# Kernel optimization log

Hardware: AMD Instinct MI355X
Metric: run time of the kernel (lower is better)

Reference implementation:

```python
import jax, jax.numpy as jnp
import numpy as np


def setup_inputs() -> dict:
    key = jax.random.key(0)
    k1, k2 = jax.random.split(key)
    b, n, d, c, h = 8, 2048, 512, 8192, 1
    x = jax.random.normal(k1, (b, n, d), dtype=jnp.float32)
    # codebook buffer: l2norm(uniform_init(h, c, d)) -- unit-norm rows
    embed = jax.random.normal(k2, (h, c, d), dtype=jnp.float32)
    embed = embed / jnp.linalg.norm(embed, axis=-1, keepdims=True)
    return {"x": x, "embed": embed}


def reference(x, embed):
    # x: [b, n, d] (ndim < 4 -> prepend codebook dim h=1); embed: [h, c, d]
    h = embed.shape[0]
    b, n, d = x.shape
    flatten = x.astype(jnp.float32).reshape(h, b * n, d)   # pack 'h * d'
    # cosine-sim scores (x assumed pre-l2-normalized via transform_input upstream)
    dist = jnp.einsum('hnd,hcd->hnc', flatten, embed)      # [h, b*n, c]
    # gumbel_sample at inference / temp->argmax: deterministic argmax over codes
    embed_ind = jnp.argmax(dist, axis=-1)                  # [h, b*n]
    ind = embed_ind.reshape(h, b, n)                       # unpack 'h *'
    # batched_embedding: gather codebook rows per index -> [h, b, n, d]
    quantize = embed[jnp.arange(h)[:, None, None], ind]
    dist = dist.reshape(h, b, n, -1)                       # unpack 'h * d'
    # needs_codebook_dim: squeeze h=1 on quantize and embed_ind (dist keeps h)
    return quantize[0], ind[0], dist
```

## Files before the change

kernel.cpp:

```cpp
#include <hip/hip_runtime.h>


#define NROWS   16384
#define NCOLS   8192
#define KDIM    512
#define KSPLIT  1024
#define NCTILES 64

#define BM 128
#define BN 128
#define BK 32
#define NSTEPS 48

typedef float f32x4 __attribute__((ext_vector_type(4)));
typedef short s16x8 __attribute__((ext_vector_type(8)));

static __device__ __forceinline__ unsigned short f2bf_rne(float f) {
    unsigned u = __float_as_uint(f);
    u = (u + 0x7FFFu + ((u >> 16) & 1u)) >> 16;
    return (unsigned short)u;
}
static __device__ __forceinline__ float bf2f(unsigned short h) {
    return __uint_as_float(((unsigned)h) << 16);
}

#define GLOAD_LDS16(g, l)                                                              \
    __builtin_amdgcn_global_load_lds((const __attribute__((address_space(1))) void*)(g), \
                                     (__attribute__((address_space(3))) void*)(l), 16, 0, 0)

__global__ __launch_bounds__(128) void split_kernel(
    const float* __restrict__ x, const float* __restrict__ embed,
    unsigned short* __restrict__ A, unsigned short* __restrict__ B)
{
    int row = blockIdx.x;
    const float* src;
    unsigned short* dst;
    if (row < NROWS) { src = x + (size_t)row * KDIM;     dst = A + (size_t)row * KSPLIT; }
    else { row -= NROWS; src = embed + (size_t)row * KDIM; dst = B + (size_t)row * KSPLIT; }

    const int t = threadIdx.x;
    const float4 v = ((const float4*)src)[t];
    const float f[4] = {v.x, v.y, v.z, v.w};
    unsigned short h[4], l[4];
#pragma unroll
    for (int i = 0; i < 4; i++) {
        h[i] = f2bf_rne(f[i]);
        l[i] = f2bf_rne(f[i] - bf2f(h[i]));
    }
    *(ushort4*)(dst + t * 4)        = make_ushort4(h[0], h[1], h[2], h[3]);
    *(ushort4*)(dst + KDIM + t * 4) = make_ushort4(l[0], l[1], l[2], l[3]);
}

__global__ __launch_bounds__(256, 3) void gemm_bf16_argmax(
    const unsigned short* __restrict__ A,
    const unsigned short* __restrict__ B,
    float* __restrict__ dist,
    float* __restrict__ ws_val,
    int*   __restrict__ ws_idx)
{
    __shared__ unsigned short As[BM * BK];
    __shared__ unsigned short Bs[BN * BK];
    __shared__ float redV[BM * 2];
    __shared__ int   redI[BM * 2];

    const int tid   = threadIdx.x;
    const int lane  = tid & 63;
    const int wid   = tid >> 6;
    const int waveM = wid >> 1;
    const int waveN = wid & 1;
    const int q     = lane >> 4;
    const int lc    = lane & 15;
    const int rowBase = blockIdx.y * BM;
    const int colBase = blockIdx.x * BN;

    const int srow   = tid >> 2;
    const int schunk = (tid & 3) * 8;
    const unsigned short* Ag = A + (size_t)(rowBase + srow) * KSPLIT + schunk;
    const unsigned short* Bg = B + (size_t)(colBase + srow) * KSPLIT + schunk;
    unsigned short* AsW = &As[tid * 8];
    unsigned short* BsW = &Bs[tid * 8];

    f32x4 acc[4][4];
#pragma unroll
    for (int m = 0; m < 4; m++)
#pragma unroll
        for (int n = 0; n < 4; n++) acc[m][n] = (f32x4){0.f, 0.f, 0.f, 0.f};

    for (int s = 0; s < NSTEPS; s++) {
        const int seg  = s >> 4;
        const int kb   = (s & 15) * BK;
        const int aOff = (seg == 1) ? KDIM : 0;
        const int bOff = (seg == 2) ? KDIM : 0;

        __syncthreads();
        GLOAD_LDS16(Ag + aOff + kb, AsW);
        GLOAD_LDS16(Ag + aOff + kb + (size_t)64 * KSPLIT, AsW + 64 * BK);
        GLOAD_LDS16(Bg + bOff + kb, BsW);
        GLOAD_LDS16(Bg + bOff + kb + (size_t)64 * KSPLIT, BsW + 64 * BK);
        __syncthreads();

        s16x8 af[4], bfr[4];
#pragma unroll
        for (int m = 0; m < 4; m++) {
            const int r = waveM * 64 + m * 16 + lc;
            af[m] = *(const s16x8*)&As[r * BK + q * 8];
        }
#pragma unroll
        for (int n = 0; n < 4; n++) {
            const int c = waveN * 64 + n * 16 + lc;
            bfr[n] = *(const s16x8*)&Bs[c * BK + q * 8];
        }
#pragma unroll
        for (int m = 0; m < 4; m++)
#pragma unroll
            for (int n = 0; n < 4; n++)
                acc[m][n] = __builtin_amdgcn_mfma_f32_16x16x32_bf16(af[m], bfr[n], acc[m][n], 0, 0, 0);
    }

#pragma unroll
    for (int m = 0; m < 4; m++) {
        const int r0 = rowBase + waveM * 64 + m * 16 + q * 4;
#pragma unroll
        for (int reg = 0; reg < 4; reg++) {
            float* dp = dist + (size_t)(r0 + reg) * NCOLS + colBase + waveN * 64 + lc;
#pragma unroll
            for (int n = 0; n < 4; n++)
                __builtin_nontemporal_store(acc[m][n][reg], dp + n * 16);
        }
    }

#pragma unroll
    for (int m = 0; m < 4; m++) {
#pragma unroll
        for (int reg = 0; reg < 4; reg++) {
            float v = acc[m][0][reg];
            int   c = colBase + waveN * 64 + lc;
#pragma unroll
            for (int n = 1; n < 4; n++) {
                const float vv = acc[m][n][reg];
                if (vv > v) { v = vv; c = colBase + waveN * 64 + n * 16 + lc; }
            }
#pragma unroll
            for (int off = 1; off < 16; off <<= 1) {
                const float ov = __shfl_xor(v, off);
                const int   oc = __shfl_xor(c, off);
                if (ov > v || (ov == v && oc < c)) { v = ov; c = oc; }
            }
            if (lc == 0) {
                const int tr = waveM * 64 + m * 16 + q * 4 + reg;
                redV[tr * 2 + waveN] = v;
                redI[tr * 2 + waveN] = c;
            }
        }
    }
    __syncthreads();

    if (tid < BM) {
        float v = redV[tid * 2]; int c = redI[tid * 2];
        const float v1 = redV[tid * 2 + 1];
        if (v1 > v) { v = v1; c = redI[tid * 2 + 1]; }
        const int r = rowBase + tid;
        ws_val[(size_t)r * NCTILES + blockIdx.x] = v;
        ws_idx[(size_t)r * NCTILES + blockIdx.x] = c;
    }
}

__global__ __launch_bounds__(256, 2) void gemm_argmax_f32(
    const float* __restrict__ x, const float* __restrict__ embed,
    float* __restrict__ dist, float* __restrict__ ws_val, int* __restrict__ ws_idx)
{
    __shared__ float As[16][BM + 4];
    __shared__ float Bs[16][BN + 4];
    __shared__ float redV[BM * 16];
    __shared__ int   redI[BM * 16];

    const int tid = threadIdx.x;
    const int tx  = tid & 15;
    const int ty  = tid >> 4;
    const int rowBase = blockIdx.y * BM;
    const int colBase = blockIdx.x * BN;
    const int lrow = tid >> 2;
    const int lc   = tid & 3;

    const float* Aptr = x     + (size_t)(rowBase + lrow) * KDIM + lc * 4;
    const float* Bptr = embed + (size_t)(colBase + lrow) * KDIM + lc * 4;

    float acc[8][8];
#pragma unroll
    for (int i = 0; i < 8; i++)
#pragma unroll
        for (int j = 0; j < 8; j++) acc[i][j] = 0.0f;

    for (int kb = 0; kb < KDIM; kb += 16) {
        const float4 a0 = *(const float4*)(Aptr + kb);
        const float4 a1 = *(const float4*)(Aptr + kb + (size_t)64 * KDIM);
        const float4 b0 = *(const float4*)(Bptr + kb);
        const float4 b1 = *(const float4*)(Bptr + kb + (size_t)64 * KDIM);
        __syncthreads();
        const int k0 = lc * 4;
        As[k0 + 0][lrow] = a0.x; As[k0 + 1][lrow] = a0.y;
        As[k0 + 2][lrow] = a0.z; As[k0 + 3][lrow] = a0.w;
        As[k0 + 0][lrow + 64] = a1.x; As[k0 + 1][lrow + 64] = a1.y;
        As[k0 + 2][lrow + 64] = a1.z; As[k0 + 3][lrow + 64] = a1.w;
        Bs[k0 + 0][lrow] = b0.x; Bs[k0 + 1][lrow] = b0.y;
        Bs[k0 + 2][lrow] = b0.z; Bs[k0 + 3][lrow] = b0.w;
        Bs[k0 + 0][lrow + 64] = b1.x; Bs[k0 + 1][lrow + 64] = b1.y;
        Bs[k0 + 2][lrow + 64] = b1.z; Bs[k0 + 3][lrow + 64] = b1.w;
        __syncthreads();
#pragma unroll
        for (int k = 0; k < 16; k++) {
            const float4 av0 = *(const float4*)&As[k][ty * 8];
            const float4 av1 = *(const float4*)&As[k][ty * 8 + 4];
            const float4 bv0 = *(const float4*)&Bs[k][tx * 8];
            const float4 bv1 = *(const float4*)&Bs[k][tx * 8 + 4];
            const float a[8] = {av0.x, av0.y, av0.z, av0.w, av1.x, av1.y, av1.z, av1.w};
            const float b[8] = {bv0.x, bv0.y, bv0.z, bv0.w, bv1.x, bv1.y, bv1.z, bv1.w};
#pragma unroll
            for (int i = 0; i < 8; i++)
#pragma unroll
                for (int j = 0; j < 8; j++)
                    acc[i][j] = fmaf(a[i], b[j], acc[i][j]);
        }
    }
#pragma unroll
    for (int i = 0; i < 8; i++) {
        const int r = rowBase + ty * 8 + i;
        float4* p = (float4*)(dist + (size_t)r * NCOLS + colBase + tx * 8);
        p[0] = make_float4(acc[i][0], acc[i][1], acc[i][2], acc[i][3]);
        p[1] = make_float4(acc[i][4], acc[i][5], acc[i][6], acc[i][7]);
    }
#pragma unroll
    for (int i = 0; i < 8; i++) {
        float bv = acc[i][0];
        int   bj = 0;
#pragma unroll
        for (int j = 1; j < 8; j++)
            if (acc[i][j] > bv) { bv = acc[i][j]; bj = j; }
        const int lrowi = ty * 8 + i;
        redV[lrowi * 16 + tx] = bv;
        redI[lrowi * 16 + tx] = colBase + tx * 8 + bj;
    }
    __syncthreads();
    if (tid < BM) {
        float bv = redV[tid * 16];
        int   bi = redI[tid * 16];
#pragma unroll
        for (int t = 1; t < 16; t++) {
            const float v = redV[tid * 16 + t];
            if (v > bv) { bv = v; bi = redI[tid * 16 + t]; }
        }
        const int r = rowBase + tid;
        ws_val[(size_t)r * NCTILES + blockIdx.x] = bv;
        ws_idx[(size_t)r * NCTILES + blockIdx.x] = bi;
    }
}

__global__ __launch_bounds__(64) void finalize_kernel(
    const float* __restrict__ ws_val,
    const int*   __restrict__ ws_idx,
    const float* __restrict__ embed,
    float* __restrict__ out_q,
    float* __restrict__ out_ind)
{
    const int r    = blockIdx.x;
    const int lane = threadIdx.x;

    float v = ws_val[(size_t)r * NCTILES + lane];
    int   i = ws_idx[(size_t)r * NCTILES + lane];

#pragma unroll
    for (int off = 32; off > 0; off >>= 1) {
        const float ov = __shfl_down(v, off);
        const int   oi = __shfl_down(i, off);
        if (ov > v || (ov == v && oi < i)) { v = ov; i = oi; }
    }
    i = __shfl(i, 0);

    if (lane == 0) out_ind[r] = (float)i;

    const float4* src = (const float4*)(embed + (size_t)i * KDIM);
    float4*       dst = (float4*)(out_q + (size_t)r * KDIM);
    dst[lane]      = src[lane];
    dst[lane + 64] = src[lane + 64];
}

extern "C" void kernel_launch(void* const* d_in, const int* in_sizes, int n_in,
                              void* d_out, int out_size, void* d_ws, size_t ws_size,
                              hipStream_t stream) {
    (void)in_sizes; (void)n_in; (void)out_size;
    const float* x     = (const float*)d_in[0];
    const float* embed = (const float*)d_in[1];

    float* out     = (float*)d_out;
    float* out_q   = out;
    float* out_ind = out + (size_t)NROWS * KDIM;
    float* dist    = out_ind + NROWS;

    const size_t abytes = (size_t)NROWS * KSPLIT * sizeof(unsigned short);
    const size_t bbytes = (size_t)NCOLS * KSPLIT * sizeof(unsigned short);
    const size_t wbytes = (size_t)NROWS * NCTILES * sizeof(float);
    const size_t wsneed = abytes + bbytes + 2 * wbytes;

    if (ws_size >= wsneed) {
        unsigned short* Asp = (unsigned short*)d_ws;
        unsigned short* Bsp = (unsigned short*)((char*)d_ws + abytes);
        float* ws_val = (float*)((char*)d_ws + abytes + bbytes);
        int*   ws_idx = (int*)((char*)d_ws + abytes + bbytes + wbytes);

        split_kernel<<<NROWS + NCOLS, 128, 0, stream>>>(x, embed, Asp, Bsp);
        gemm_bf16_argmax<<<dim3(NCOLS / BN, NROWS / BM), 256, 0, stream>>>(
            Asp, Bsp, dist, ws_val, ws_idx);
        finalize_kernel<<<dim3(NROWS), dim3(64), 0, stream>>>(ws_val, ws_idx, embed, out_q, out_ind);
    } else {
        float* ws_val = (float*)d_ws;
        int*   ws_idx = (int*)((char*)d_ws + wbytes);
        gemm_argmax_f32<<<dim3(NCOLS / 128, NROWS / 128), 256, 0, stream>>>(
            x, embed, dist, ws_val, ws_idx);
        finalize_kernel<<<dim3(NROWS), dim3(64), 0, stream>>>(ws_val, ws_idx, embed, out_q, out_ind);
    }
}
```

Before: 971.4 us.

## Double-buffer bf16x3 GEMM with XOR-swizzled LDS and hi/lo fused k-steps

Replaces the single-buffered 48-step bf16 split GEMM with a double-buffered pipeline. Each stage loads 64 columns (hi and lo halves of a 32-wide k-chunk) into XOR-swizzled LDS, and the loop waits on vmcnt so the next stage's global->LDS loads overlap the MFMAs. The hi fragments are reused across the hi*hi, hi*lo and lo*hi products, which cuts LDS reads and barriers per k-step. Tile order is swizzled for L2 locality and s_setprio is raised around the MFMA bursts. The cost is doubled LDS per block, with occupancy dropped to 2 blocks per SIMD, and reliance on exact manual waitcnt counts.

```diff
diff --git a/kernel.cpp b/kernel.cpp
--- a/kernel.cpp
+++ b/kernel.cpp
@@ -9,8 +9,6 @@
 
 #define BM 128
 #define BN 128
-#define BK 32
-#define NSTEPS 48
 
 typedef float f32x4 __attribute__((ext_vector_type(4)));
 typedef short s16x8 __attribute__((ext_vector_type(8)));
@@ -51,15 +49,65 @@
     *(ushort4*)(dst + KDIM + t * 4) = make_ushort4(l[0], l[1], l[2], l[3]);
 }
 
-__global__ __launch_bounds__(256, 3) void gemm_bf16_argmax(
+
+#define STAGE(S, BUF) do {                                            \
+    const int kb_ = (S) * 32;                                         \
+    GLOAD_LDS16(Ag0 + kb_,              &As[BUF][t8]);                \
+    GLOAD_LDS16(Ag0 + kb_ + 32*KSPLIT,  &As[BUF][t8 + 2048]);         \
+    GLOAD_LDS16(Ag0 + kb_ + 64*KSPLIT,  &As[BUF][t8 + 4096]);         \
+    GLOAD_LDS16(Ag0 + kb_ + 96*KSPLIT,  &As[BUF][t8 + 6144]);         \
+    GLOAD_LDS16(Bg0 + kb_,              &Bs[BUF][t8]);                \
+    GLOAD_LDS16(Bg0 + kb_ + 32*KSPLIT,  &Bs[BUF][t8 + 2048]);         \
+    GLOAD_LDS16(Bg0 + kb_ + 64*KSPLIT,  &Bs[BUF][t8 + 4096]);         \
+    GLOAD_LDS16(Bg0 + kb_ + 96*KSPLIT,  &Bs[BUF][t8 + 6144]);         \
+} while (0)
+
+#define COMPUTE(BUF) do {                                                              \
+    s16x8 afh[4], bfh[4], bfl[4], afl[4];                                              \
+    _Pragma("unroll")                                                                  \
+    for (int m = 0; m < 4; m++)                                                        \
+        afh[m] = *(const s16x8*)&As[BUF][(waveM*64 + m*16 + lc)*64 + sh];              \
+    _Pragma("unroll")                                                                  \
+    for (int n = 0; n < 4; n++)                                                        \
+        bfh[n] = *(const s16x8*)&Bs[BUF][(waveN*64 + n*16 + lc)*64 + sh];              \
+    __builtin_amdgcn_s_setprio(1);                                                     \
+    _Pragma("unroll")                                                                  \
+    for (int m = 0; m < 4; m++)                                                        \
+        _Pragma("unroll")                                                              \
+        for (int n = 0; n < 4; n++)                                                    \
+            acc[m][n] = __builtin_amdgcn_mfma_f32_16x16x32_bf16(afh[m], bfh[n], acc[m][n], 0, 0, 0); \
+    __builtin_amdgcn_s_setprio(0);                                                     \
+    _Pragma("unroll")                                                                  \
+    for (int n = 0; n < 4; n++)                                                        \
+        bfl[n] = *(const s16x8*)&Bs[BUF][(waveN*64 + n*16 + lc)*64 + sl];              \
+    __builtin_amdgcn_s_setprio(1);                                                     \
+    _Pragma("unroll")                                                                  \
+    for (int m = 0; m < 4; m++)                                                        \
+        _Pragma("unroll")                                                              \
+        for (int n = 0; n < 4; n++)                                                    \
+            acc[m][n] = __builtin_amdgcn_mfma_f32_16x16x32_bf16(afh[m], bfl[n], acc[m][n], 0, 0, 0); \
+    __builtin_amdgcn_s_setprio(0);                                                     \
+    _Pragma("unroll")                                                                  \
+    for (int m = 0; m < 4; m++)                                                        \
+        afl[m] = *(const s16x8*)&As[BUF][(waveM*64 + m*16 + lc)*64 + sl];              \
+    __builtin_amdgcn_s_setprio(1);                                                     \
+    _Pragma("unroll")                                                                  \
+    for (int m = 0; m < 4; m++)                                                        \
+        _Pragma("unroll")                                                              \
+        for (int n = 0; n < 4; n++)                                                    \
+            acc[m][n] = __builtin_amdgcn_mfma_f32_16x16x32_bf16(afl[m], bfh[n], acc[m][n], 0, 0, 0); \
+    __builtin_amdgcn_s_setprio(0);                                                     \
+} while (0)
+
+__global__ __launch_bounds__(256, 2) void gemm_bf16_pipe(
     const unsigned short* __restrict__ A,
     const unsigned short* __restrict__ B,
     float* __restrict__ dist,
     float* __restrict__ ws_val,
     int*   __restrict__ ws_idx)
 {
-    __shared__ unsigned short As[BM * BK];
-    __shared__ unsigned short Bs[BN * BK];
+    __shared__ unsigned short As[2][BM * 64];
+    __shared__ unsigned short Bs[2][BN * 64];
     __shared__ float redV[BM * 2];
     __shared__ int   redI[BM * 2];
 
@@ -70,15 +118,22 @@
     const int waveN = wid & 1;
     const int q     = lane >> 4;
     const int lc    = lane & 15;
-    const int rowBase = blockIdx.y * BM;
-    const int colBase = blockIdx.x * BN;
-
-    const int srow   = tid >> 2;
-    const int schunk = (tid & 3) * 8;
-    const unsigned short* Ag = A + (size_t)(rowBase + srow) * KSPLIT + schunk;
-    const unsigned short* Bg = B + (size_t)(colBase + srow) * KSPLIT + schunk;
-    unsigned short* AsW = &As[tid * 8];
-    unsigned short* BsW = &Bs[tid * 8];
+
+    const int fid = blockIdx.y * 64 + blockIdx.x;
+    const int swz = (fid & 7) * 1024 + (fid >> 3);
+    const int bx  = swz & 63;
+    const int by  = swz >> 6;
+    const int rowBase = by * BM;
+    const int colBase = bx * BN;
+
+    const int g    = (tid & 7) ^ ((tid >> 3) & 7);
+    const int goff = (g >> 2) * 512 + (g & 3) * 8;
+    const unsigned short* Ag0 = A + (size_t)(rowBase + (tid >> 3)) * KSPLIT + goff;
+    const unsigned short* Bg0 = B + (size_t)(colBase + (tid >> 3)) * KSPLIT + goff;
+    const int t8 = tid * 8;
+
+    const int sh = ((q        ^ (lc & 7)) << 3);
+    const int sl = (((q | 4)  ^ (lc & 7)) << 3);
 
     f32x4 acc[4][4];
 #pragma unroll
@@ -86,35 +141,29 @@
 #pragma unroll
         for (int n = 0; n < 4; n++) acc[m][n] = (f32x4){0.f, 0.f, 0.f, 0.f};
 
-    for (int s = 0; s < NSTEPS; s++) {
-        const int seg  = s >> 4;
-        const int kb   = (s & 15) * BK;
-        const int aOff = (seg == 1) ? KDIM : 0;
-        const int bOff = (seg == 2) ? KDIM : 0;
-
-        __syncthreads();
-        GLOAD_LDS16(Ag + aOff + kb, AsW);
-        GLOAD_LDS16(Ag + aOff + kb + (size_t)64 * KSPLIT, AsW + 64 * BK);
-        GLOAD_LDS16(Bg + bOff + kb, BsW);
-        GLOAD_LDS16(Bg + bOff + kb + (size_t)64 * KSPLIT, BsW + 64 * BK);
-        __syncthreads();
-
-        s16x8 af[4], bfr[4];
-#pragma unroll
-        for (int m = 0; m < 4; m++) {
-            const int r = waveM * 64 + m * 16 + lc;
-            af[m] = *(const s16x8*)&As[r * BK + q * 8];
-        }
-#pragma unroll
-        for (int n = 0; n < 4; n++) {
-            const int c = waveN * 64 + n * 16 + lc;
-            bfr[n] = *(const s16x8*)&Bs[c * BK + q * 8];
-        }
-#pragma unroll
-        for (int m = 0; m < 4; m++)
-#pragma unroll
-            for (int n = 0; n < 4; n++)
-                acc[m][n] = __builtin_amdgcn_mfma_f32_16x16x32_bf16(af[m], bfr[n], acc[m][n], 0, 0, 0);
+    STAGE(0, 0);
+
+#pragma unroll 1
+    for (int s = 0; s < 16; s += 2) {
+        STAGE(s + 1, 1);
+        asm volatile("s_waitcnt vmcnt(8)" ::: "memory");
+        __builtin_amdgcn_s_barrier();
+        asm volatile("" ::: "memory");
+        COMPUTE(0);
+        asm volatile("" ::: "memory");
+        __builtin_amdgcn_s_barrier();
+
+        if (s + 2 < 16) {
+            STAGE(s + 2, 0);
+            asm volatile("s_waitcnt vmcnt(8)" ::: "memory");
+        } else {
+            asm volatile("s_waitcnt vmcnt(0)" ::: "memory");
+        }
+        __builtin_amdgcn_s_barrier();
+        asm volatile("" ::: "memory");
+        COMPUTE(1);
+        asm volatile("" ::: "memory");
+        __builtin_amdgcn_s_barrier();
     }
 
 #pragma unroll
@@ -160,8 +209,8 @@
         const float v1 = redV[tid * 2 + 1];
         if (v1 > v) { v = v1; c = redI[tid * 2 + 1]; }
         const int r = rowBase + tid;
-        ws_val[(size_t)r * NCTILES + blockIdx.x] = v;
-        ws_idx[(size_t)r * NCTILES + blockIdx.x] = c;
+        ws_val[(size_t)r * NCTILES + bx] = v;
+        ws_idx[(size_t)r * NCTILES + bx] = c;
     }
 }
 
@@ -308,7 +357,7 @@
         int*   ws_idx = (int*)((char*)d_ws + abytes + bbytes + wbytes);
 
         split_kernel<<<NROWS + NCOLS, 128, 0, stream>>>(x, embed, Asp, Bsp);
-        gemm_bf16_argmax<<<dim3(NCOLS / BN, NROWS / BM), 256, 0, stream>>>(
+        gemm_bf16_pipe<<<dim3(NCOLS / BN, NROWS / BM), 256, 0, stream>>>(
             Asp, Bsp, dist, ws_val, ws_idx);
         finalize_kernel<<<dim3(NROWS), dim3(64), 0, stream>>>(ws_val, ws_idx, embed, out_q, out_ind);
     } else {
```

Result: no change. 966.5 us (-0.5%).

## Rewrite bf16x3 GEMM as 256x256 double-buffered 8-wave kernel with swizzled LDS

Applied to the files above, without the earlier changes.

Replaces the 128x128 single-buffered split-bf16 GEMM with a 256x256 tile, 512-thread kernel. It loads the hi and lo halves of each k-slice together into XOR-swizzled, double-buffered LDS and runs the three MFMA products per slice in four phases. Global-to-LDS prefetch of the next slice overlaps the MFMAs, with barriers and s_setprio around the MFMA phases. The larger tile halves the number of column tiles, so the finalize kernel now takes a tile count. The change raises LDS use and register pressure (32 accumulators per wave) and relies on hand-placed waitcnt and barriers.

```diff
diff --git a/kernel.cpp b/kernel.cpp
--- a/kernel.cpp
+++ b/kernel.cpp
@@ -5,12 +5,11 @@
 #define NCOLS   8192
 #define KDIM    512
 #define KSPLIT  1024
-#define NCTILES 64
-
-#define BM 128
-#define BN 128
-#define BK 32
-#define NSTEPS 48
+
+#define BM 256
+#define BN 256
+#define NCTILES 32
+#define NKT 16
 
 typedef float f32x4 __attribute__((ext_vector_type(4)));
 typedef short s16x8 __attribute__((ext_vector_type(8)));
@@ -51,75 +50,138 @@
     *(ushort4*)(dst + KDIM + t * 4) = make_ushort4(l[0], l[1], l[2], l[3]);
 }
 
-__global__ __launch_bounds__(256, 3) void gemm_bf16_argmax(
+
+#define STAGE_A(T, BUF) do { const int kb_ = (T) * 32;                      \
+    GLOAD_LDS16(Ag0 + kb_,                    &As[BUF][tid * 8]);           \
+    GLOAD_LDS16(Ag0 + kb_ +  64 * KSPLIT,     &As[BUF][tid * 8 + 4096]);    \
+    GLOAD_LDS16(Ag0 + kb_ + 128 * KSPLIT,     &As[BUF][tid * 8 + 8192]);    \
+    GLOAD_LDS16(Ag0 + kb_ + 192 * KSPLIT,     &As[BUF][tid * 8 + 12288]);   \
+} while (0)
+#define STAGE_B(T, BUF) do { const int kb_ = (T) * 32;                      \
+    GLOAD_LDS16(Bg0 + kb_,                    &Bs[BUF][tid * 8]);           \
+    GLOAD_LDS16(Bg0 + kb_ +  64 * KSPLIT,     &Bs[BUF][tid * 8 + 4096]);    \
+    GLOAD_LDS16(Bg0 + kb_ + 128 * KSPLIT,     &Bs[BUF][tid * 8 + 8192]);    \
+    GLOAD_LDS16(Bg0 + kb_ + 192 * KSPLIT,     &Bs[BUF][tid * 8 + 12288]);   \
+} while (0)
+
+#define LOAD_A(M0) do {                                                          \
+    ah[0] = *(const s16x8*)&Ac[(waveM * 128 + ((M0) + 0) * 16 + lc) * 64 + sh];  \
+    al[0] = *(const s16x8*)&Ac[(waveM * 128 + ((M0) + 0) * 16 + lc) * 64 + sl];  \
+    ah[1] = *(const s16x8*)&Ac[(waveM * 128 + ((M0) + 1) * 16 + lc) * 64 + sh];  \
+    al[1] = *(const s16x8*)&Ac[(waveM * 128 + ((M0) + 1) * 16 + lc) * 64 + sl];  \
+} while (0)
+
+#define PHASE_MFMA(M0) do {                                                      \
+    _Pragma("unroll")                                                            \
+    for (int mm = 0; mm < 2; mm++) {                                             \
+        _Pragma("unroll")                                                        \
+        for (int n = 0; n < 4; n++)                                              \
+            acc[(M0) + mm][n] = __builtin_amdgcn_mfma_f32_16x16x32_bf16(         \
+                ah[mm], bh[n], acc[(M0) + mm][n], 0, 0, 0);                      \
+        _Pragma("unroll")                                                        \
+        for (int n = 0; n < 4; n++)                                              \
+            acc[(M0) + mm][n] = __builtin_amdgcn_mfma_f32_16x16x32_bf16(         \
+                ah[mm], bl[n], acc[(M0) + mm][n], 0, 0, 0);                      \
+        _Pragma("unroll")                                                        \
+        for (int n = 0; n < 4; n++)                                              \
+            acc[(M0) + mm][n] = __builtin_amdgcn_mfma_f32_16x16x32_bf16(         \
+                al[mm], bh[n], acc[(M0) + mm][n], 0, 0, 0);                      \
+    }                                                                            \
+} while (0)
+
+#define PHASE_SYNC_PRE()  do { __builtin_amdgcn_s_barrier();                      \
+    asm volatile("s_waitcnt lgkmcnt(0)" ::: "memory");                            \
+    __builtin_amdgcn_s_setprio(1); } while (0)
+#define PHASE_SYNC_POST() do { __builtin_amdgcn_s_setprio(0);                     \
+    asm volatile("" ::: "memory");                                                \
+    __builtin_amdgcn_s_barrier(); } while (0)
+
+__global__ __launch_bounds__(512, 2) void gemm_bf16_8phase(
     const unsigned short* __restrict__ A,
     const unsigned short* __restrict__ B,
     float* __restrict__ dist,
     float* __restrict__ ws_val,
     int*   __restrict__ ws_idx)
 {
-    __shared__ unsigned short As[BM * BK];
-    __shared__ unsigned short Bs[BN * BK];
-    __shared__ float redV[BM * 2];
-    __shared__ int   redI[BM * 2];
+    __shared__ unsigned short As[2][BM * 64];
+    __shared__ unsigned short Bs[2][BN * 64];
+    __shared__ float redV[BM * 4];
+    __shared__ int   redI[BM * 4];
 
     const int tid   = threadIdx.x;
     const int lane  = tid & 63;
     const int wid   = tid >> 6;
-    const int waveM = wid >> 1;
-    const int waveN = wid & 1;
+    const int waveM = wid >> 2;
+    const int waveN = wid & 3;
     const int q     = lane >> 4;
     const int lc    = lane & 15;
+
     const int rowBase = blockIdx.y * BM;
     const int colBase = blockIdx.x * BN;
 
-    const int srow   = tid >> 2;
-    const int schunk = (tid & 3) * 8;
-    const unsigned short* Ag = A + (size_t)(rowBase + srow) * KSPLIT + schunk;
-    const unsigned short* Bg = B + (size_t)(colBase + srow) * KSPLIT + schunk;
-    unsigned short* AsW = &As[tid * 8];
-    unsigned short* BsW = &Bs[tid * 8];
-
-    f32x4 acc[4][4];
-#pragma unroll
-    for (int m = 0; m < 4; m++)
+    const int srow = tid >> 3;
+    const int g    = (tid & 7) ^ (srow & 7);
+    const int goff = (g >> 2) * 512 + (g & 3) * 8;
+    const unsigned short* Ag0 = A + (size_t)(rowBase + srow) * KSPLIT + goff;
+    const unsigned short* Bg0 = B + (size_t)(colBase + srow) * KSPLIT + goff;
+
+    const int sh = ((q       ^ (lc & 7)) << 3);
+    const int sl = (((q | 4) ^ (lc & 7)) << 3);
+
+    f32x4 acc[8][4];
+#pragma unroll
+    for (int m = 0; m < 8; m++)
 #pragma unroll
         for (int n = 0; n < 4; n++) acc[m][n] = (f32x4){0.f, 0.f, 0.f, 0.f};
 
-    for (int s = 0; s < NSTEPS; s++) {
-        const int seg  = s >> 4;
-        const int kb   = (s & 15) * BK;
-        const int aOff = (seg == 1) ? KDIM : 0;
-        const int bOff = (seg == 2) ? KDIM : 0;
-
-        __syncthreads();
-        GLOAD_LDS16(Ag + aOff + kb, AsW);
-        GLOAD_LDS16(Ag + aOff + kb + (size_t)64 * KSPLIT, AsW + 64 * BK);
-        GLOAD_LDS16(Bg + bOff + kb, BsW);
-        GLOAD_LDS16(Bg + bOff + kb + (size_t)64 * KSPLIT, BsW + 64 * BK);
-        __syncthreads();
-
-        s16x8 af[4], bfr[4];
-#pragma unroll
-        for (int m = 0; m < 4; m++) {
-            const int r = waveM * 64 + m * 16 + lc;
-            af[m] = *(const s16x8*)&As[r * BK + q * 8];
-        }
+    STAGE_A(0, 0);
+    STAGE_B(0, 0);
+    asm volatile("s_waitcnt vmcnt(0)" ::: "memory");
+    __builtin_amdgcn_s_barrier();
+
+#pragma unroll 1
+    for (int t = 0; t < NKT; t++) {
+        const int cur = t & 1, nxt = cur ^ 1;
+        const unsigned short* Ac = &As[cur][0];
+        const unsigned short* Bc = &Bs[cur][0];
+        s16x8 bh[4], bl[4], ah[2], al[2];
+
 #pragma unroll
         for (int n = 0; n < 4; n++) {
-            const int c = waveN * 64 + n * 16 + lc;
-            bfr[n] = *(const s16x8*)&Bs[c * BK + q * 8];
-        }
-#pragma unroll
-        for (int m = 0; m < 4; m++)
-#pragma unroll
-            for (int n = 0; n < 4; n++)
-                acc[m][n] = __builtin_amdgcn_mfma_f32_16x16x32_bf16(af[m], bfr[n], acc[m][n], 0, 0, 0);
-    }
-
-#pragma unroll
-    for (int m = 0; m < 4; m++) {
-        const int r0 = rowBase + waveM * 64 + m * 16 + q * 4;
+            bh[n] = *(const s16x8*)&Bc[(waveN * 64 + n * 16 + lc) * 64 + sh];
+            bl[n] = *(const s16x8*)&Bc[(waveN * 64 + n * 16 + lc) * 64 + sl];
+        }
+        LOAD_A(0);
+        if (t + 1 < NKT) STAGE_A(t + 1, nxt);
+        PHASE_SYNC_PRE();
+        PHASE_MFMA(0);
+        PHASE_SYNC_POST();
+
+        LOAD_A(2);
+        if (t + 1 < NKT) STAGE_B(t + 1, nxt);
+        PHASE_SYNC_PRE();
+        PHASE_MFMA(2);
+        PHASE_SYNC_POST();
+
+        LOAD_A(4);
+        PHASE_SYNC_PRE();
+        PHASE_MFMA(4);
+        PHASE_SYNC_POST();
+
+        LOAD_A(6);
+        __builtin_amdgcn_s_barrier();
+        asm volatile("s_waitcnt lgkmcnt(0)" ::: "memory");
+        __builtin_amdgcn_s_setprio(1);
+        PHASE_MFMA(6);
+        __builtin_amdgcn_s_setprio(0);
+        if (t + 1 < NKT) asm volatile("s_waitcnt vmcnt(0)" ::: "memory");
+        asm volatile("" ::: "memory");
+        __builtin_amdgcn_s_barrier();
+    }
+
+#pragma unroll
+    for (int m = 0; m < 8; m++) {
+        const int r0 = rowBase + waveM * 128 + m * 16 + q * 4;
 #pragma unroll
         for (int reg = 0; reg < 4; reg++) {
             float* dp = dist + (size_t)(r0 + reg) * NCOLS + colBase + waveN * 64 + lc;
@@ -130,7 +192,7 @@
     }
 
 #pragma unroll
-    for (int m = 0; m < 4; m++) {
+    for (int m = 0; m < 8; m++) {
 #pragma unroll
         for (int reg = 0; reg < 4; reg++) {
             float v = acc[m][0][reg];
@@ -147,38 +209,42 @@
                 if (ov > v || (ov == v && oc < c)) { v = ov; c = oc; }
             }
             if (lc == 0) {
-                const int tr = waveM * 64 + m * 16 + q * 4 + reg;
-                redV[tr * 2 + waveN] = v;
-                redI[tr * 2 + waveN] = c;
+                const int tr = waveM * 128 + m * 16 + q * 4 + reg;
+                redV[tr * 4 + waveN] = v;
+                redI[tr * 4 + waveN] = c;
             }
         }
     }
     __syncthreads();
 
     if (tid < BM) {
-        float v = redV[tid * 2]; int c = redI[tid * 2];
-        const float v1 = redV[tid * 2 + 1];
-        if (v1 > v) { v = v1; c = redI[tid * 2 + 1]; }
+        float v = redV[tid * 4]; int c = redI[tid * 4];
+#pragma unroll
+        for (int w = 1; w < 4; w++) {
+            const float vv = redV[tid * 4 + w];
+            if (vv > v) { v = vv; c = redI[tid * 4 + w]; }
+        }
         const int r = rowBase + tid;
         ws_val[(size_t)r * NCTILES + blockIdx.x] = v;
         ws_idx[(size_t)r * NCTILES + blockIdx.x] = c;
     }
 }
 
+#define FB_NCT 64
 __global__ __launch_bounds__(256, 2) void gemm_argmax_f32(
     const float* __restrict__ x, const float* __restrict__ embed,
     float* __restrict__ dist, float* __restrict__ ws_val, int* __restrict__ ws_idx)
 {
-    __shared__ float As[16][BM + 4];
-    __shared__ float Bs[16][BN + 4];
-    __shared__ float redV[BM * 16];
-    __shared__ int   redI[BM * 16];
+    __shared__ float As[16][128 + 4];
+    __shared__ float Bs[16][128 + 4];
+    __shared__ float redV[128 * 16];
+    __shared__ int   redI[128 * 16];
 
     const int tid = threadIdx.x;
     const int tx  = tid & 15;
     const int ty  = tid >> 4;
-    const int rowBase = blockIdx.y * BM;
-    const int colBase = blockIdx.x * BN;
+    const int rowBase = blockIdx.y * 128;
+    const int colBase = blockIdx.x * 128;
     const int lrow = tid >> 2;
     const int lc   = tid & 3;
 
@@ -241,7 +307,7 @@
         redI[lrowi * 16 + tx] = colBase + tx * 8 + bj;
     }
     __syncthreads();
-    if (tid < BM) {
+    if (tid < 128) {
         float bv = redV[tid * 16];
         int   bi = redI[tid * 16];
 #pragma unroll
@@ -250,8 +316,8 @@
             if (v > bv) { bv = v; bi = redI[tid * 16 + t]; }
         }
         const int r = rowBase + tid;
-        ws_val[(size_t)r * NCTILES + blockIdx.x] = bv;
-        ws_idx[(size_t)r * NCTILES + blockIdx.x] = bi;
+        ws_val[(size_t)r * FB_NCT + blockIdx.x] = bv;
+        ws_idx[(size_t)r * FB_NCT + blockIdx.x] = bi;
     }
 }
 
@@ -260,13 +326,20 @@
     const int*   __restrict__ ws_idx,
     const float* __restrict__ embed,
     float* __restrict__ out_q,
-    float* __restrict__ out_ind)
+    float* __restrict__ out_ind,
+    int ntiles)
 {
     const int r    = blockIdx.x;
     const int lane = threadIdx.x;
 
-    float v = ws_val[(size_t)r * NCTILES + lane];
-    int   i = ws_idx[(size_t)r * NCTILES + lane];
+    float v; int i;
+    if (lane < ntiles) {
+        v = ws_val[(size_t)r * ntiles + lane];
+        i = ws_idx[(size_t)r * ntiles + lane];
+    } else {
+        v = -__builtin_inff();
+        i = 0x7FFFFFFF;
+    }
 
 #pragma unroll
     for (int off = 32; off > 0; off >>= 1) {
@@ -308,14 +381,16 @@
         int*   ws_idx = (int*)((char*)d_ws + abytes + bbytes + wbytes);
 
         split_kernel<<<NROWS + NCOLS, 128, 0, stream>>>(x, embed, Asp, Bsp);
-        gemm_bf16_argmax<<<dim3(NCOLS / BN, NROWS / BM), 256, 0, stream>>>(
+        gemm_bf16_8phase<<<dim3(NCOLS / BN, NROWS / BM), 512, 0, stream>>>(
             Asp, Bsp, dist, ws_val, ws_idx);
-        finalize_kernel<<<dim3(NROWS), dim3(64), 0, stream>>>(ws_val, ws_idx, embed, out_q, out_ind);
+        finalize_kernel<<<dim3(NROWS), dim3(64), 0, stream>>>(
+            ws_val, ws_idx, embed, out_q, out_ind, NCTILES);
     } else {
         float* ws_val = (float*)d_ws;
-        int*   ws_idx = (int*)((char*)d_ws + wbytes);
+        int*   ws_idx = (int*)((char*)d_ws + (size_t)NROWS * FB_NCT * sizeof(float));
         gemm_argmax_f32<<<dim3(NCOLS / 128, NROWS / 128), 256, 0, stream>>>(
             x, embed, dist, ws_val, ws_idx);
-        finalize_kernel<<<dim3(NROWS), dim3(64), 0, stream>>>(ws_val, ws_idx, embed, out_q, out_ind);
-    }
-}
+        finalize_kernel<<<dim3(NROWS), dim3(64), 0, stream>>>(
+            ws_val, ws_idx, embed, out_q, out_ind, FB_NCT);
+    }
+}
```

Result: faster. 926.0 us (-4.7%).
